# Kernel optimization log

Measured on AMD Instinct MI355X. Metric: run time of the kernel, lower is better.

## Reference

```python
import jax, jax.numpy as jnp
import numpy as np

D_MODEL = 1024
NUM_HEADS = 16
SEQ = 2048
BATCH = 4
THETA = 10000.0
D_K = D_MODEL // NUM_HEADS


def setup_inputs() -> dict:
    key = jax.random.key(0)
    k1, k2, k3, k4, k5 = jax.random.split(key, 5)
    std = np.sqrt(2.0 / (D_MODEL + D_MODEL))
    x = jax.random.normal(k1, (BATCH, SEQ, D_MODEL), dtype=jnp.float32)
    wq = jax.random.normal(k2, (D_MODEL, D_MODEL), dtype=jnp.float32) * std
    wk = jax.random.normal(k3, (D_MODEL, D_MODEL), dtype=jnp.float32) * std
    wv = jax.random.normal(k4, (D_MODEL, D_MODEL), dtype=jnp.float32) * std
    wo = jax.random.normal(k5, (D_MODEL, D_MODEL), dtype=jnp.float32) * std
    token_positions = jnp.arange(SEQ, dtype=jnp.int32)
    return {"x": x, "wq": wq, "wk": wk, "wv": wv, "wo": wo,
            "token_positions": token_positions}


def _apply_rope(t, cos, sin):
    # t: (b, h, s, d_k); cos/sin: (s, d_k/2) -> broadcast over (b, h)
    pairs = t.reshape(*t.shape[:-1], D_K // 2, 2)
    x0, x1 = pairs[..., 0], pairs[..., 1]
    r0 = x0 * cos - x1 * sin
    r1 = x0 * sin + x1 * cos
    return jnp.stack((r0, r1), axis=-1).reshape(t.shape)


def reference(x, wq, wk, wv, wo, token_positions):
    b, s, d = x.shape
    h, dk = NUM_HEADS, D_K

    def split_heads(y):  # (b, s, d) -> (b, h, s, d_k)
        return y.reshape(b, s, h, dk).transpose(0, 2, 1, 3)

    q = split_heads(x @ wq.T)
    k = split_heads(x @ wk.T)
    v = split_heads(x @ wv.T)

    # RoPE tables: angles_j = theta^{-(2j)/d_k}, j = 0..d_k/2-1
    inv_freq = 1.0 / (THETA ** (jnp.arange(0, dk, 2, dtype=jnp.float32) / dk))
    ang = token_positions.astype(jnp.float32)[:, None] * inv_freq[None, :]  # (s, d_k/2)
    cos, sin = jnp.cos(ang), jnp.sin(ang)
    q = _apply_rope(q, cos, sin)
    k = _apply_rope(k, cos, sin)

    scores = jnp.einsum('bhqd,bhkd->bhqk', q, k) / jnp.sqrt(jnp.float32(dk))
    causal = jnp.tril(jnp.ones((s, s), dtype=bool))
    scores = jnp.where(causal, scores, -jnp.inf)
    attn = jax.nn.softmax(scores, axis=-1)
    out = jnp.einsum('bhqk,bhkd->bhqd', attn, v)  # (b, h, s, d_k)
    out = out.transpose(0, 2, 1, 3).reshape(b, s, d)
    return out @ wo.T
```

## Files before the change

### kernel.cpp

```cpp
#include <hip/hip_runtime.h>
#include <stdint.h>

#define B_   4
#define S_   2048
#define H_   16
#define DK_  64
#define DM_  1024
#define M_   (B_ * S_)

typedef __attribute__((ext_vector_type(4)))  float f32x4;
typedef __attribute__((ext_vector_type(16))) float f32x16;
typedef __attribute__((ext_vector_type(8)))  short s16x8;

#define SCQ 0.18033688011112042f

__device__ __forceinline__ uint16_t f2bf(float f) {
    union { float f; uint32_t u; } v; v.f = f;
    uint32_t u = v.u;
    uint32_t r = (u + 0x7FFFu + ((u >> 16) & 1u)) >> 16;
    return (uint16_t)r;
}
__device__ __forceinline__ float bf2f(uint16_t h) {
    union { uint32_t u; float f; } v; v.u = ((uint32_t)h) << 16;
    return v.f;
}
__device__ __forceinline__ uint32_t cvt_pk_bf16(float lo, float hi) {
    uint32_t r;
    asm("v_cvt_pk_bf16_f32 %0, %1, %2" : "=v"(r) : "v"(lo), "v"(hi));
    return r;
}

__device__ __forceinline__ void gload_lds16(const uint16_t* g, uint16_t* l) {
    __builtin_amdgcn_global_load_lds(
        (const __attribute__((address_space(1))) void*)g,
        (__attribute__((address_space(3))) void*)l, 16, 0, 0);
}

__global__ __launch_bounds__(256) void cvt_all(const float* __restrict__ x,
                                               const float* __restrict__ w0,
                                               const float* __restrict__ w1,
                                               const float* __restrict__ w2,
                                               const float* __restrict__ w3,
                                               uint16_t* __restrict__ xo,
                                               uint16_t* __restrict__ o0,
                                               uint16_t* __restrict__ o1,
                                               uint16_t* __restrict__ o2,
                                               uint16_t* __restrict__ o3) {
    const size_t NX = (size_t)M_ * DM_;
    const size_t NW = (size_t)DM_ * DM_;
    size_t i = ((size_t)blockIdx.x * 256 + threadIdx.x) * 4;
    const float* in; uint16_t* out; size_t off;
    if (i < NX) { in = x; out = xo; off = i; }
    else {
        size_t j = i - NX;
        int sel = (int)(j >> 20);
        off = j & (NW - 1);
        in  = sel == 0 ? w0 : sel == 1 ? w1 : sel == 2 ? w2 : w3;
        out = sel == 0 ? o0 : sel == 1 ? o1 : sel == 2 ? o2 : o3;
    }
    float4 v = *reinterpret_cast<const float4*>(in + off);
    ushort4 o;
    o.x = f2bf(v.x); o.y = f2bf(v.y); o.z = f2bf(v.z); o.w = f2bf(v.w);
    *reinterpret_cast<ushort4*>(out + off) = o;
}

__global__ __launch_bounds__(256, 4) void gemm_qkv(const uint16_t* __restrict__ xb,
                                                   const uint16_t* __restrict__ wq,
                                                   const uint16_t* __restrict__ wk,
                                                   const uint16_t* __restrict__ wv,
                                                   uint16_t* __restrict__ qout,
                                                   uint16_t* __restrict__ kout,
                                                   uint16_t* __restrict__ vout) {
    __shared__ uint16_t Al[2][128 * 32];
    __shared__ uint16_t Bl[2][128 * 32];
    const int K = DM_;
    const int lane = threadIdx.x & 63;
    const int w    = threadIdx.x >> 6;
    const int wr   = w >> 1, wc = w & 1;
    const int sel  = blockIdx.x >> 3;
    const int np   = blockIdx.x & 7;
    const int y    = blockIdx.y;
    const int ql   = lane & 31;
    const int hi   = lane >> 5;

    const uint16_t* Aptr; const uint16_t* Bptr;
    int m0, n0;
    if (sel == 2) { Aptr = wv; Bptr = xb; m0 = np * 128; n0 = y * 128; }
    else          { Aptr = xb; Bptr = sel ? wk : wq; m0 = y * 128; n0 = np * 128; }

    const int srow = w * 32 + (lane >> 2);
    const int scol = (((lane & 3) ^ ((lane >> 3) & 3))) * 8;
    const uint16_t* Ag = Aptr + (size_t)(m0 + srow) * K + scol;
    const uint16_t* Bg = Bptr + (size_t)(n0 + srow) * K + scol;
    const int loff = w * 32 * 32;
    const int qsw  = (ql >> 1) & 3;

    f32x16 acc[2][2] = {};
#pragma unroll
    for (int i = 0; i < 2; ++i) {
        gload_lds16(Ag + (size_t)i * 16 * K, &Al[0][loff + i * 16 * 32]);
        gload_lds16(Bg + (size_t)i * 16 * K, &Bl[0][loff + i * 16 * 32]);
    }

    int cur = 0;
    for (int k0 = 0; k0 < K; k0 += 32) {
        __syncthreads();
        if (k0 + 32 < K) {
            const int nb = cur ^ 1, k2 = k0 + 32;
#pragma unroll
            for (int i = 0; i < 2; ++i) {
                gload_lds16(Ag + (size_t)i * 16 * K + k2, &Al[nb][loff + i * 16 * 32]);
                gload_lds16(Bg + (size_t)i * 16 * K + k2, &Bl[nb][loff + i * 16 * 32]);
            }
        }
        s16x8 af[2][2], bfr[2][2];
#pragma unroll
        for (int am = 0; am < 2; ++am)
#pragma unroll
            for (int ks = 0; ks < 2; ++ks)
                af[am][ks] = *reinterpret_cast<const s16x8*>(
                    &Al[cur][(wr * 64 + am * 32 + ql) * 32 + (((ks * 2 + hi) ^ qsw) * 8)]);
#pragma unroll
        for (int bn = 0; bn < 2; ++bn)
#pragma unroll
            for (int ks = 0; ks < 2; ++ks)
                bfr[bn][ks] = *reinterpret_cast<const s16x8*>(
                    &Bl[cur][(wc * 64 + bn * 32 + ql) * 32 + (((ks * 2 + hi) ^ qsw) * 8)]);
#pragma unroll
        for (int am = 0; am < 2; ++am)
#pragma unroll
            for (int bn = 0; bn < 2; ++bn) {
                acc[am][bn] = __builtin_amdgcn_mfma_f32_32x32x16_bf16(af[am][0], bfr[bn][0],
                                                                      acc[am][bn], 0, 0, 0);
                acc[am][bn] = __builtin_amdgcn_mfma_f32_32x32x16_bf16(af[am][1], bfr[bn][1],
                                                                      acc[am][bn], 0, 0, 0);
            }
        cur ^= 1;
    }

#pragma unroll
    for (int am = 0; am < 2; ++am)
#pragma unroll
        for (int bn = 0; bn < 2; ++bn)
#pragma unroll
            for (int r = 0; r < 16; ++r) {
                const int cr = (r & 3) + 8 * (r >> 2);
                int row = m0 + wr * 64 + am * 32 + 4 * hi + cr;
                int col = n0 + wc * 64 + bn * 32 + ql;
                float v = acc[am][bn][r];
                if (sel == 2) {
                    int h = row >> 6,  dk = row & 63;
                    int b = col >> 11, s = col & (S_ - 1);
                    vout[(((size_t)(b * H_ + h)) * DK_ + dk) * S_ + s] = f2bf(v);
                } else {
                    int b = row >> 11, s = row & (S_ - 1);
                    int h = col >> 6,  dk = col & 63;
                    uint16_t bv = f2bf(sel ? v : v * SCQ);
                    (sel ? kout : qout)[(((size_t)(b * H_ + h)) * S_ + s) * DK_ + dk] = bv;
                }
            }
}

__global__ __launch_bounds__(256, 4) void gemm_out(const uint16_t* __restrict__ A,
                                                   const uint16_t* __restrict__ Bm,
                                                   float* __restrict__ Cout,
                                                   int M, int N, int K) {
    __shared__ uint16_t Al[2][128 * 32];
    __shared__ uint16_t Bl[2][128 * 32];
    const int lane = threadIdx.x & 63;
    const int w    = threadIdx.x >> 6;
    const int wr   = w >> 1, wc = w & 1;
    const int m0   = blockIdx.x * 128;
    const int n0   = blockIdx.y * 128;
    const int ql   = lane & 31;
    const int hi   = lane >> 5;

    const int srow = w * 32 + (lane >> 2);
    const int scol = (((lane & 3) ^ ((lane >> 3) & 3))) * 8;
    const uint16_t* Ag = A  + (size_t)(m0 + srow) * K + scol;
    const uint16_t* Bg = Bm + (size_t)(n0 + srow) * K + scol;
    const int loff = w * 32 * 32;
    const int qsw  = (ql >> 1) & 3;

    f32x16 acc[2][2] = {};
#pragma unroll
    for (int i = 0; i < 2; ++i) {
        gload_lds16(Ag + (size_t)i * 16 * K, &Al[0][loff + i * 16 * 32]);
        gload_lds16(Bg + (size_t)i * 16 * K, &Bl[0][loff + i * 16 * 32]);
    }

    int cur = 0;
    for (int k0 = 0; k0 < K; k0 += 32) {
        __syncthreads();
        if (k0 + 32 < K) {
            const int nb = cur ^ 1, k2 = k0 + 32;
#pragma unroll
            for (int i = 0; i < 2; ++i) {
                gload_lds16(Ag + (size_t)i * 16 * K + k2, &Al[nb][loff + i * 16 * 32]);
                gload_lds16(Bg + (size_t)i * 16 * K + k2, &Bl[nb][loff + i * 16 * 32]);
            }
        }
        s16x8 af[2][2], bfr[2][2];
#pragma unroll
        for (int am = 0; am < 2; ++am)
#pragma unroll
            for (int ks = 0; ks < 2; ++ks)
                af[am][ks] = *reinterpret_cast<const s16x8*>(
                    &Al[cur][(wr * 64 + am * 32 + ql) * 32 + (((ks * 2 + hi) ^ qsw) * 8)]);
#pragma unroll
        for (int bn = 0; bn < 2; ++bn)
#pragma unroll
            for (int ks = 0; ks < 2; ++ks)
                bfr[bn][ks] = *reinterpret_cast<const s16x8*>(
                    &Bl[cur][(wc * 64 + bn * 32 + ql) * 32 + (((ks * 2 + hi) ^ qsw) * 8)]);
#pragma unroll
        for (int am = 0; am < 2; ++am)
#pragma unroll
            for (int bn = 0; bn < 2; ++bn) {
                acc[am][bn] = __builtin_amdgcn_mfma_f32_32x32x16_bf16(af[am][0], bfr[bn][0],
                                                                      acc[am][bn], 0, 0, 0);
                acc[am][bn] = __builtin_amdgcn_mfma_f32_32x32x16_bf16(af[am][1], bfr[bn][1],
                                                                      acc[am][bn], 0, 0, 0);
            }
        cur ^= 1;
    }

#pragma unroll
    for (int am = 0; am < 2; ++am)
#pragma unroll
        for (int bn = 0; bn < 2; ++bn)
#pragma unroll
            for (int r = 0; r < 16; ++r) {
                const int cr = (r & 3) + 8 * (r >> 2);
                int row = m0 + wr * 64 + am * 32 + 4 * hi + cr;
                int col = n0 + wc * 64 + bn * 32 + ql;
                Cout[(size_t)row * N + col] = acc[am][bn][r];
            }
}

__global__ __launch_bounds__(256) void rope_kernel(uint16_t* __restrict__ a,
                                                   const int* __restrict__ pos,
                                                   int npairs) {
    int t = blockIdx.x * 256 + threadIdx.x;
    if (t >= npairs) return;
    int j = t & 31;
    int s = (t >> 5) & (S_ - 1);
    float p   = (float)pos[s];
    float inv = exp2f(-(float)j * (13.287712379549449f / 32.0f));
    float ang = p * inv;
    float sn = __sinf(ang);
    float c  = __cosf(ang);
    uint32_t pr = *reinterpret_cast<uint32_t*>(a + (size_t)2 * t);
    float x0 = bf2f((uint16_t)(pr & 0xFFFF));
    float x1 = bf2f((uint16_t)(pr >> 16));
    float r0 = x0 * c - x1 * sn;
    float r1 = x0 * sn + x1 * c;
    uint32_t ot = (uint32_t)f2bf(r0) | ((uint32_t)f2bf(r1) << 16);
    *reinterpret_cast<uint32_t*>(a + (size_t)2 * t) = ot;
}

__global__ __launch_bounds__(256, 2) void flash_attn(const uint16_t* __restrict__ qg,
                                                     const uint16_t* __restrict__ kg,
                                                     const uint16_t* __restrict__ vtg,
                                                     const int* __restrict__ tpos,
                                                     uint16_t* __restrict__ attn) {
    __shared__ __align__(16) uint16_t Kl[2][2][4096];
    __shared__ __align__(16) uint16_t Vl[2][2][4096];
    const int lane = threadIdx.x & 63;
    const int w    = threadIdx.x >> 6;
    const int ql   = lane & 31;
    const int hi   = lane >> 5;
    const int id   = blockIdx.x;
    const int bh   = (id & 7) * 8 + ((id >> 3) & 7);
    const int s    = 15 - (id >> 6);
    const int b    = bh >> 4, hh = bh & 15;

    const uint16_t* kb_ = kg  + (size_t)bh * S_ * DK_;
    const uint16_t* vb_ = vtg + (size_t)bh * DK_ * S_;

    char* obb = (char*)&Kl[0][0][0] + w * 4096;
    const int swz = (ql & 7) << 4;

    const int q0 = s * 128 + w * 32;
    const int rowg  = q0 + ql;
    const int ntmax = 2 * s + 2;

    const int srow = lane >> 3;
    const int scol = ((lane & 7) ^ srow) << 3;

    const uint16_t* qp = qg + ((size_t)bh * S_ + q0 + ql) * DK_ + hi * 8;
    const float prow = (float)tpos[rowg];
    const float FR = 13.287712379549449f / 32.0f;
    s16x8 qf[4];
#pragma unroll
    for (int kk = 0; kk < 4; ++kk) {
        s16x8 raw = *reinterpret_cast<const s16x8*>(qp + kk * 16);
        union { uint32_t u[4]; s16x8 v; } pw;
#pragma unroll
        for (int jj = 0; jj < 4; ++jj) {
            float x0 = bf2f((uint16_t)raw[2 * jj]);
            float x1 = bf2f((uint16_t)raw[2 * jj + 1]);
            float ang = prow * exp2f(-(float)(kk * 8 + hi * 4 + jj) * FR);
            float sn = __sinf(ang), cs = __cosf(ang);
            pw.u[jj] = cvt_pk_bf16(x0 * cs - x1 * sn, x0 * sn + x1 * cs);
        }
        qf[kk] = pw.v;
    }

    f32x16 o0 = {}, o1 = {};
    float l_l = 0.f;

    auto do_tile = [&](int kt, const uint16_t* Kh, const uint16_t* Vh) {
        if (kt > q0 + 31) return;

        s16x8 kf[8];
#pragma unroll
        for (int kb2 = 0; kb2 < 2; ++kb2)
#pragma unroll
            for (int kk = 0; kk < 4; ++kk)
                kf[kb2 * 4 + kk] = *reinterpret_cast<const s16x8*>(
                    &Kh[(kb2 * 32 + ql) * 64 + (((kk * 32 + hi * 16) ^ swz) >> 1)]);

        f32x16 sc0 = {}, sc1 = {};
        __builtin_amdgcn_s_setprio(1);
#pragma unroll
        for (int kk = 0; kk < 4; ++kk)
            sc0 = __builtin_amdgcn_mfma_f32_32x32x16_bf16(kf[kk], qf[kk], sc0, 0, 0, 0);
#pragma unroll
        for (int kk = 0; kk < 4; ++kk)
            sc1 = __builtin_amdgcn_mfma_f32_32x32x16_bf16(kf[4 + kk], qf[kk], sc1, 0, 0, 0);
        __builtin_amdgcn_s_setprio(0);

        if (kt + 63 > q0) {
            const int keybase = kt + 4 * hi;
#pragma unroll
            for (int r = 0; r < 16; ++r) {
                const int cr = (r & 3) + 8 * (r >> 2);
                if (keybase + cr > rowg)      sc0[r] = -3e38f;
                if (keybase + cr + 32 > rowg) sc1[r] = -3e38f;
            }
        }

#pragma unroll
        for (int r = 0; r < 16; ++r) {
            float p0 = exp2f(sc0[r]);
            float p1 = exp2f(sc1[r]);
            sc0[r] = p0; sc1[r] = p1;
            l_l += p0 + p1;
        }

        s16x8 pf[4];
        {
            union PW { uint32_t u[4]; s16x8 v; };
#pragma unroll
            for (int half = 0; half < 2; ++half) {
                const f32x16& e = half ? sc1 : sc0;
#pragma unroll
                for (int sl = 0; sl < 2; ++sl) {
                    const int rb = sl * 8;
                    uint32_t a0 = cvt_pk_bf16(e[rb + 0], e[rb + 1]);
                    uint32_t b0 = cvt_pk_bf16(e[rb + 4], e[rb + 5]);
                    uint32_t a1 = cvt_pk_bf16(e[rb + 2], e[rb + 3]);
                    uint32_t b1 = cvt_pk_bf16(e[rb + 6], e[rb + 7]);
                    asm("v_permlane32_swap_b32 %0, %1" : "+v"(a0), "+v"(b0));
                    asm("v_permlane32_swap_b32 %0, %1" : "+v"(a1), "+v"(b1));
                    PW pw; pw.u[0] = a0; pw.u[1] = a1; pw.u[2] = b0; pw.u[3] = b1;
                    pf[half * 2 + sl] = pw.v;
                }
            }
        }

        s16x8 vf[8];
#pragma unroll
        for (int db = 0; db < 2; ++db)
#pragma unroll
            for (int ks = 0; ks < 4; ++ks)
                vf[db * 4 + ks] = *reinterpret_cast<const s16x8*>(
                    &Vh[(db * 32 + ql) * 64 + (((ks * 32 + hi * 16) ^ swz) >> 1)]);

        __builtin_amdgcn_s_setprio(1);
#pragma unroll
        for (int ks = 0; ks < 4; ++ks) {
            o0 = __builtin_amdgcn_mfma_f32_32x32x16_bf16(vf[ks],     pf[ks], o0, 0, 0, 0);
            o1 = __builtin_amdgcn_mfma_f32_32x32x16_bf16(vf[4 + ks], pf[ks], o1, 0, 0, 0);
        }
        __builtin_amdgcn_s_setprio(0);
    };

#pragma unroll
    for (int half = 0; half < 2; ++half) {
        const int kt2 = half * 64;
#pragma unroll
        for (int i = 0; i < 2; ++i) {
            gload_lds16(kb_ + (size_t)(kt2 + w * 16 + i * 8 + srow) * DK_ + scol,
                        &Kl[0][half][w * 1024 + i * 512]);
            gload_lds16(vb_ + (size_t)(w * 16 + i * 8 + srow) * S_ + kt2 + scol,
                        &Vl[0][half][w * 1024 + i * 512]);
        }
    }

    for (int t = 0; t < ntmax; t += 2) {
        const int cur = (t >> 1) & 1;
        __syncthreads();
        if (t + 2 < ntmax) {
            const int nb = cur ^ 1;
#pragma unroll
            for (int half = 0; half < 2; ++half) {
                const int kt2 = (t + 2 + half) * 64;
#pragma unroll
                for (int i = 0; i < 2; ++i) {
                    gload_lds16(kb_ + (size_t)(kt2 + w * 16 + i * 8 + srow) * DK_ + scol,
                                &Kl[nb][half][w * 1024 + i * 512]);
                    gload_lds16(vb_ + (size_t)(w * 16 + i * 8 + srow) * S_ + kt2 + scol,
                                &Vl[nb][half][w * 1024 + i * 512]);
                }
            }
        }
        do_tile(t * 64,       &Kl[cur][0][0], &Vl[cur][0][0]);
        do_tile((t + 1) * 64, &Kl[cur][1][0], &Vl[cur][1][0]);
    }

    __syncthreads();

    l_l += __shfl_xor(l_l, 32);
    float rinv = 1.0f / l_l;

#pragma unroll
    for (int db = 0; db < 2; ++db) {
        const f32x16& o = db ? o1 : o0;
#pragma unroll
        for (int rq = 0; rq < 4; ++rq) {
            uint2 val;
            val.x = cvt_pk_bf16(o[4 * rq + 0] * rinv, o[4 * rq + 1] * rinv);
            val.y = cvt_pk_bf16(o[4 * rq + 2] * rinv, o[4 * rq + 3] * rinv);
            int colb = (db * 32 + 8 * rq + 4 * hi) * 2;
            *reinterpret_cast<uint2*>(obb + ql * 128 + (colb ^ swz)) = val;
        }
    }
    uint16_t* orow = attn + ((size_t)b * S_ + q0 + ql) * DM_ + hh * 64 + hi * 32;
#pragma unroll
    for (int i = 0; i < 4; ++i) {
        int colb = hi * 64 + i * 16;
        s16x8 vrow = *reinterpret_cast<const s16x8*>(obb + ql * 128 + (colb ^ swz));
        *reinterpret_cast<s16x8*>(orow + i * 8) = vrow;
    }
}

extern "C" void kernel_launch(void* const* d_in, const int* in_sizes, int n_in,
                              void* d_out, int out_size, void* d_ws, size_t ws_size,
                              hipStream_t stream) {
    (void)in_sizes; (void)n_in; (void)out_size;
    const float* x   = (const float*)d_in[0];
    const float* wq  = (const float*)d_in[1];
    const float* wk  = (const float*)d_in[2];
    const float* wv  = (const float*)d_in[3];
    const float* wo  = (const float*)d_in[4];
    const int* tpos  = (const int*)d_in[5];
    float* out = (float*)d_out;

    const size_t NX = (size_t)M_ * DM_;
    const size_t NW = (size_t)DM_ * DM_;
    const size_t need = (NX + 4 * NW + 4 * NX) * sizeof(uint16_t);
    if (ws_size < need) return;

    uint16_t* ws  = (uint16_t*)d_ws;
    uint16_t* xb  = ws;
    uint16_t* wqb = xb + NX;
    uint16_t* wkb = wqb + NW;
    uint16_t* wvb = wkb + NW;
    uint16_t* wob = wvb + NW;
    uint16_t* qb  = wob + NW;
    uint16_t* kb  = qb + NX;
    uint16_t* vtb = kb + NX;
    uint16_t* ab  = vtb + NX;

    cvt_all<<<(int)((NX + 4 * NW) / 1024), 256, 0, stream>>>(x, wq, wk, wv, wo,
                                                             xb, wqb, wkb, wvb, wob);

    gemm_qkv<<<dim3(24, M_ / 128), 256, 0, stream>>>(xb, wqb, wkb, wvb, qb, kb, vtb);

    int npairs_k = B_ * H_ * S_ * (DK_ / 2);
    rope_kernel<<<npairs_k / 256, 256, 0, stream>>>(kb, tpos, npairs_k);

    flash_attn<<<dim3(1024), 256, 0, stream>>>(qb, kb, vtb, tpos, ab);

    gemm_out<<<dim3(M_ / 128, DM_ / 128), 256, 0, stream>>>(ab, wob, out, M_, DM_, DM_);
}
```

Measured before the change: 193.6 us.

## Process 64 query rows per wave to reuse K/V fragments, zigzag block order

Each wave in the flash attention kernel now handles two 32-row query groups (64 rows) instead of one. The K and V fragments loaded from LDS are shared across both groups, which halves LDS traffic per MFMA, and the grid is halved to 512 blocks. Query blocks are assigned in a zigzag order so heavy and light causal blocks are interleaved. In exchange, register pressure roughly doubles for accumulators and scores, which could cost occupancy under the 2-blocks-per-CU launch bound. The larger blocks also make the causal workload coarser and less even across CUs.

```diff
diff --git a/kernel.cpp b/kernel.cpp
--- a/kernel.cpp
+++ b/kernel.cpp
@@ -272,7 +272,8 @@
     const int hi   = lane >> 5;
     const int id   = blockIdx.x;
     const int bh   = (id & 7) * 8 + ((id >> 3) & 7);
-    const int s    = 15 - (id >> 6);
+    const int zig  = id >> 6;
+    const int ss   = (zig < 4) ? (7 - zig) : (zig - 4);
     const int b    = bh >> 4, hh = bh & 15;
 
     const uint16_t* kb_ = kg  + (size_t)bh * S_ * DK_;
@@ -281,37 +282,47 @@
     char* obb = (char*)&Kl[0][0][0] + w * 4096;
     const int swz = (ql & 7) << 4;
 
-    const int q0 = s * 128 + w * 32;
-    const int rowg  = q0 + ql;
-    const int ntmax = 2 * s + 2;
+    const int q0 = ss * 256 + w * 64;
+    const int rowA  = q0 + ql;
+    const int rowB  = q0 + 32 + ql;
+    const int ntmax = 4 * ss + 4;
 
     const int srow = lane >> 3;
     const int scol = ((lane & 7) ^ srow) << 3;
 
-    const uint16_t* qp = qg + ((size_t)bh * S_ + q0 + ql) * DK_ + hi * 8;
-    const float prow = (float)tpos[rowg];
     const float FR = 13.287712379549449f / 32.0f;
-    s16x8 qf[4];
-#pragma unroll
-    for (int kk = 0; kk < 4; ++kk) {
-        s16x8 raw = *reinterpret_cast<const s16x8*>(qp + kk * 16);
-        union { uint32_t u[4]; s16x8 v; } pw;
-#pragma unroll
-        for (int jj = 0; jj < 4; ++jj) {
-            float x0 = bf2f((uint16_t)raw[2 * jj]);
-            float x1 = bf2f((uint16_t)raw[2 * jj + 1]);
-            float ang = prow * exp2f(-(float)(kk * 8 + hi * 4 + jj) * FR);
-            float sn = __sinf(ang), cs = __cosf(ang);
-            pw.u[jj] = cvt_pk_bf16(x0 * cs - x1 * sn, x0 * sn + x1 * cs);
-        }
-        qf[kk] = pw.v;
-    }
-
-    f32x16 o0 = {}, o1 = {};
-    float l_l = 0.f;
+    s16x8 qfA[4], qfB[4];
+    {
+        const uint16_t* qpA = qg + ((size_t)bh * S_ + rowA) * DK_ + hi * 8;
+        const uint16_t* qpB = qg + ((size_t)bh * S_ + rowB) * DK_ + hi * 8;
+        const float pA = (float)tpos[rowA];
+        const float pB = (float)tpos[rowB];
+#pragma unroll
+        for (int kk = 0; kk < 4; ++kk) {
+            s16x8 rawA = *reinterpret_cast<const s16x8*>(qpA + kk * 16);
+            s16x8 rawB = *reinterpret_cast<const s16x8*>(qpB + kk * 16);
+            union { uint32_t u[4]; s16x8 v; } pwA, pwB;
+#pragma unroll
+            for (int jj = 0; jj < 4; ++jj) {
+                float inv = exp2f(-(float)(kk * 8 + hi * 4 + jj) * FR);
+                float aA = pA * inv, aB = pB * inv;
+                float snA = __sinf(aA), csA = __cosf(aA);
+                float snB = __sinf(aB), csB = __cosf(aB);
+                float a0 = bf2f((uint16_t)rawA[2 * jj]), a1 = bf2f((uint16_t)rawA[2 * jj + 1]);
+                float b0 = bf2f((uint16_t)rawB[2 * jj]), b1 = bf2f((uint16_t)rawB[2 * jj + 1]);
+                pwA.u[jj] = cvt_pk_bf16(a0 * csA - a1 * snA, a0 * snA + a1 * csA);
+                pwB.u[jj] = cvt_pk_bf16(b0 * csB - b1 * snB, b0 * snB + b1 * csB);
+            }
+            qfA[kk] = pwA.v;
+            qfB[kk] = pwB.v;
+        }
+    }
+
+    f32x16 oA0 = {}, oA1 = {}, oB0 = {}, oB1 = {};
+    float lA = 0.f, lB = 0.f;
 
     auto do_tile = [&](int kt, const uint16_t* Kh, const uint16_t* Vh) {
-        if (kt > q0 + 31) return;
+        if (kt > q0 + 63) return;
 
         s16x8 kf[8];
 #pragma unroll
@@ -321,14 +332,15 @@
                 kf[kb2 * 4 + kk] = *reinterpret_cast<const s16x8*>(
                     &Kh[(kb2 * 32 + ql) * 64 + (((kk * 32 + hi * 16) ^ swz) >> 1)]);
 
-        f32x16 sc0 = {}, sc1 = {};
+        f32x16 sA0 = {}, sA1 = {}, sB0 = {}, sB1 = {};
         __builtin_amdgcn_s_setprio(1);
 #pragma unroll
-        for (int kk = 0; kk < 4; ++kk)
-            sc0 = __builtin_amdgcn_mfma_f32_32x32x16_bf16(kf[kk], qf[kk], sc0, 0, 0, 0);
-#pragma unroll
-        for (int kk = 0; kk < 4; ++kk)
-            sc1 = __builtin_amdgcn_mfma_f32_32x32x16_bf16(kf[4 + kk], qf[kk], sc1, 0, 0, 0);
+        for (int kk = 0; kk < 4; ++kk) {
+            sA0 = __builtin_amdgcn_mfma_f32_32x32x16_bf16(kf[kk],     qfA[kk], sA0, 0, 0, 0);
+            sA1 = __builtin_amdgcn_mfma_f32_32x32x16_bf16(kf[4 + kk], qfA[kk], sA1, 0, 0, 0);
+            sB0 = __builtin_amdgcn_mfma_f32_32x32x16_bf16(kf[kk],     qfB[kk], sB0, 0, 0, 0);
+            sB1 = __builtin_amdgcn_mfma_f32_32x32x16_bf16(kf[4 + kk], qfB[kk], sB1, 0, 0, 0);
+        }
         __builtin_amdgcn_s_setprio(0);
 
         if (kt + 63 > q0) {
@@ -336,36 +348,42 @@
 #pragma unroll
             for (int r = 0; r < 16; ++r) {
                 const int cr = (r & 3) + 8 * (r >> 2);
-                if (keybase + cr > rowg)      sc0[r] = -3e38f;
-                if (keybase + cr + 32 > rowg) sc1[r] = -3e38f;
+                if (keybase + cr > rowA)      sA0[r] = -3e38f;
+                if (keybase + cr + 32 > rowA) sA1[r] = -3e38f;
+                if (keybase + cr > rowB)      sB0[r] = -3e38f;
+                if (keybase + cr + 32 > rowB) sB1[r] = -3e38f;
             }
         }
 
 #pragma unroll
         for (int r = 0; r < 16; ++r) {
-            float p0 = exp2f(sc0[r]);
-            float p1 = exp2f(sc1[r]);
-            sc0[r] = p0; sc1[r] = p1;
-            l_l += p0 + p1;
-        }
-
-        s16x8 pf[4];
+            float a0 = exp2f(sA0[r]), a1 = exp2f(sA1[r]);
+            float b0 = exp2f(sB0[r]), b1 = exp2f(sB1[r]);
+            sA0[r] = a0; sA1[r] = a1; sB0[r] = b0; sB1[r] = b1;
+            lA += a0 + a1;
+            lB += b0 + b1;
+        }
+
+        s16x8 pfA[4], pfB[4];
         {
             union PW { uint32_t u[4]; s16x8 v; };
 #pragma unroll
-            for (int half = 0; half < 2; ++half) {
-                const f32x16& e = half ? sc1 : sc0;
-#pragma unroll
-                for (int sl = 0; sl < 2; ++sl) {
-                    const int rb = sl * 8;
-                    uint32_t a0 = cvt_pk_bf16(e[rb + 0], e[rb + 1]);
-                    uint32_t b0 = cvt_pk_bf16(e[rb + 4], e[rb + 5]);
-                    uint32_t a1 = cvt_pk_bf16(e[rb + 2], e[rb + 3]);
-                    uint32_t b1 = cvt_pk_bf16(e[rb + 6], e[rb + 7]);
-                    asm("v_permlane32_swap_b32 %0, %1" : "+v"(a0), "+v"(b0));
-                    asm("v_permlane32_swap_b32 %0, %1" : "+v"(a1), "+v"(b1));
-                    PW pw; pw.u[0] = a0; pw.u[1] = a1; pw.u[2] = b0; pw.u[3] = b1;
-                    pf[half * 2 + sl] = pw.v;
+            for (int g = 0; g < 2; ++g) {
+#pragma unroll
+                for (int half = 0; half < 2; ++half) {
+                    const f32x16& e = g ? (half ? sB1 : sB0) : (half ? sA1 : sA0);
+#pragma unroll
+                    for (int sl = 0; sl < 2; ++sl) {
+                        const int rb = sl * 8;
+                        uint32_t a0 = cvt_pk_bf16(e[rb + 0], e[rb + 1]);
+                        uint32_t b0 = cvt_pk_bf16(e[rb + 4], e[rb + 5]);
+                        uint32_t a1 = cvt_pk_bf16(e[rb + 2], e[rb + 3]);
+                        uint32_t b1 = cvt_pk_bf16(e[rb + 6], e[rb + 7]);
+                        asm("v_permlane32_swap_b32 %0, %1" : "+v"(a0), "+v"(b0));
+                        asm("v_permlane32_swap_b32 %0, %1" : "+v"(a1), "+v"(b1));
+                        PW pw; pw.u[0] = a0; pw.u[1] = a1; pw.u[2] = b0; pw.u[3] = b1;
+                        (g ? pfB : pfA)[half * 2 + sl] = pw.v;
+                    }
                 }
             }
         }
@@ -381,8 +399,10 @@
         __builtin_amdgcn_s_setprio(1);
 #pragma unroll
         for (int ks = 0; ks < 4; ++ks) {
-            o0 = __builtin_amdgcn_mfma_f32_32x32x16_bf16(vf[ks],     pf[ks], o0, 0, 0, 0);
-            o1 = __builtin_amdgcn_mfma_f32_32x32x16_bf16(vf[4 + ks], pf[ks], o1, 0, 0, 0);
+            oA0 = __builtin_amdgcn_mfma_f32_32x32x16_bf16(vf[ks],     pfA[ks], oA0, 0, 0, 0);
+            oA1 = __builtin_amdgcn_mfma_f32_32x32x16_bf16(vf[4 + ks], pfA[ks], oA1, 0, 0, 0);
+            oB0 = __builtin_amdgcn_mfma_f32_32x32x16_bf16(vf[ks],     pfB[ks], oB0, 0, 0, 0);
+            oB1 = __builtin_amdgcn_mfma_f32_32x32x16_bf16(vf[4 + ks], pfB[ks], oB1, 0, 0, 0);
         }
         __builtin_amdgcn_s_setprio(0);
     };
@@ -422,27 +442,33 @@
 
     __syncthreads();
 
-    l_l += __shfl_xor(l_l, 32);
-    float rinv = 1.0f / l_l;
-
-#pragma unroll
-    for (int db = 0; db < 2; ++db) {
-        const f32x16& o = db ? o1 : o0;
-#pragma unroll
-        for (int rq = 0; rq < 4; ++rq) {
-            uint2 val;
-            val.x = cvt_pk_bf16(o[4 * rq + 0] * rinv, o[4 * rq + 1] * rinv);
-            val.y = cvt_pk_bf16(o[4 * rq + 2] * rinv, o[4 * rq + 3] * rinv);
-            int colb = (db * 32 + 8 * rq + 4 * hi) * 2;
-            *reinterpret_cast<uint2*>(obb + ql * 128 + (colb ^ swz)) = val;
-        }
-    }
-    uint16_t* orow = attn + ((size_t)b * S_ + q0 + ql) * DM_ + hh * 64 + hi * 32;
-#pragma unroll
-    for (int i = 0; i < 4; ++i) {
-        int colb = hi * 64 + i * 16;
-        s16x8 vrow = *reinterpret_cast<const s16x8*>(obb + ql * 128 + (colb ^ swz));
-        *reinterpret_cast<s16x8*>(orow + i * 8) = vrow;
+    lA += __shfl_xor(lA, 32);
+    lB += __shfl_xor(lB, 32);
+    const float rinvA = 1.0f / lA;
+    const float rinvB = 1.0f / lB;
+
+#pragma unroll
+    for (int g = 0; g < 2; ++g) {
+        const float rinv = g ? rinvB : rinvA;
+#pragma unroll
+        for (int db = 0; db < 2; ++db) {
+            const f32x16& o = g ? (db ? oB1 : oB0) : (db ? oA1 : oA0);
+#pragma unroll
+            for (int rq = 0; rq < 4; ++rq) {
+                uint2 val;
+                val.x = cvt_pk_bf16(o[4 * rq + 0] * rinv, o[4 * rq + 1] * rinv);
+                val.y = cvt_pk_bf16(o[4 * rq + 2] * rinv, o[4 * rq + 3] * rinv);
+                int colb = (db * 32 + 8 * rq + 4 * hi) * 2;
+                *reinterpret_cast<uint2*>(obb + ql * 128 + (colb ^ swz)) = val;
+            }
+        }
+        uint16_t* orow = attn + ((size_t)b * S_ + q0 + g * 32 + ql) * DM_ + hh * 64 + hi * 32;
+#pragma unroll
+        for (int i = 0; i < 4; ++i) {
+            int colb = hi * 64 + i * 16;
+            s16x8 vrow = *reinterpret_cast<const s16x8*>(obb + ql * 128 + (colb ^ swz));
+            *reinterpret_cast<s16x8*>(orow + i * 8) = vrow;
+        }
     }
 }
 
@@ -482,7 +508,7 @@
     int npairs_k = B_ * H_ * S_ * (DK_ / 2);
     rope_kernel<<<npairs_k / 256, 256, 0, stream>>>(kb, tpos, npairs_k);
 
-    flash_attn<<<dim3(1024), 256, 0, stream>>>(qb, kb, vtb, tpos, ab);
+    flash_attn<<<dim3(512), 256, 0, stream>>>(qb, kb, vtb, tpos, ab);
 
     gemm_out<<<dim3(M_ / 128, DM_ / 128), 256, 0, stream>>>(ab, wob, out, M_, DM_, DM_);
 }
```

Result: no change. 193.8 us (+0.1%).
